# Performance work log

Hardware: AMD Instinct MI355X
Metric: run time of the kernel (lower is better)

Reference implementation:

```python
import jax, jax.numpy as jnp
import numpy as np
import math

B, S = 2, 2048
D_IN = 512
D_OUT = 512
P = 8
K = 8


def setup_inputs() -> dict:
    key = jax.random.key(0)
    ks = jax.random.split(key, 8)
    mean_phi = math.log(math.sqrt(2.0 / (D_IN * K)))
    mean_w2 = math.log(math.sqrt(2.0 / D_OUT))
    x = jax.random.normal(ks[0], (B, S, D_IN), dtype=jnp.float32)
    phi_raw = mean_phi + 0.2 * jax.random.normal(ks[1], (D_OUT, D_IN * K), dtype=jnp.float32)
    phi_bias = jnp.zeros((D_OUT,), dtype=jnp.float32)
    raw_weight2 = mean_w2 + 0.2 * jax.random.normal(ks[2], (P, D_OUT, D_OUT), dtype=jnp.float32)
    bias2 = jnp.zeros((P, D_OUT), dtype=jnp.float32)
    gate_raw2 = jnp.full((P,), -3.0, dtype=jnp.float32)
    # kaiming_uniform with a=sqrt(5) on shape (P, 2*D_in, D_out): fan_in = 2*D_in
    bound = math.sqrt(6.0 / ((1.0 + 5.0) * (2 * D_IN)))
    z_weight = jax.random.uniform(ks[3], (P, 2 * D_IN, D_OUT), dtype=jnp.float32,
                                  minval=-bound, maxval=bound)
    gate_raw = jnp.full((P,), -3.0, dtype=jnp.float32)
    output_bias = jnp.zeros((P, D_OUT), dtype=jnp.float32)
    return {
        "x": x, "phi_raw": phi_raw, "phi_bias": phi_bias,
        "raw_weight2": raw_weight2, "bias2": bias2, "gate_raw2": gate_raw2,
        "z_weight": z_weight, "gate_raw": gate_raw, "output_bias": output_bias,
    }


def reference(x, phi_raw, phi_bias, raw_weight2, bias2, gate_raw2,
              z_weight, gate_raw, output_bias):
    sp = jax.nn.softplus
    orig = x.shape
    x_flat = x.reshape(-1, D_IN)                              # [N, Din]
    N = x_flat.shape[0]
    shifts = jnp.linspace(-1.0, 1.0, K, dtype=x.dtype)        # [k]
    phi = sp(x_flat[:, :, None] + shifts[None, None, :])      # [N, Din, k]
    phi_flat = phi.reshape(N, D_IN * K)                       # [N, Din*k]
    # PositiveLinearHK: weight = softplus(raw)^2
    w_phi = jnp.square(sp(phi_raw))                           # [Dout, Din*k]
    x_proj = phi_flat @ w_phi.T + phi_bias                    # [N, Dout]
    g1 = jax.nn.sigmoid(gate_raw)[:, None, None]              # [P,1,1]
    z0 = sp(x_proj[None, :, :] * g1)                          # [P, N, Dout]
    w2 = jnp.square(sp(raw_weight2))                          # [P, Dout, Dout]
    # bmm(z0, w2.transpose(1,2)) == einsum over the second Dout axis of w2
    z1 = jnp.einsum('pnd,ped->pne', z0, w2) + bias2[:, None, :]
    g2 = jax.nn.sigmoid(gate_raw2)[:, None, None]
    z1 = sp(z1 * g2)                                          # [P, N, Dout]
    x_res_in = jnp.concatenate([x_flat, x_flat], axis=-1)     # [N, 2*Din]
    x_res = jnp.einsum('nc,pce->pne', x_res_in, z_weight)     # [P, N, Dout]
    z_final = sp(z1 + x_res) + output_bias[:, None, :]        # [P, N, Dout]
    out = jnp.transpose(z_final, (1, 0, 2))                   # [N, P, Dout]
    return out.reshape(tuple(orig[:-1]) + (P, D_OUT))
```

## Files before the change

### kernel.cpp

```cpp
#include <hip/hip_runtime.h>

typedef unsigned short u16;
typedef __attribute__((ext_vector_type(8))) short bf16x8;
typedef __attribute__((ext_vector_type(4))) float floatx4;
typedef __attribute__((ext_vector_type(8))) unsigned short u16x8;
typedef __attribute__((ext_vector_type(4))) unsigned short u16x4;

#define NTOK 4096
#define DDIN 512
#define DDOUT 512
#define NP 8
#define SPLITK 8

__device__ __forceinline__ float b2f(u16 b) {
    union { unsigned int u; float f; } v; v.u = ((unsigned int)b) << 16; return v.f;
}
__device__ __forceinline__ u16 f2b(float f) {
    union { float f; unsigned int u; } v; v.f = f;
    unsigned int r = (v.u + 0x7fffu + ((v.u >> 16) & 1u)) >> 16;
    return (u16)r;
}
__device__ __forceinline__ float sp(float x) {
    return fmaxf(x, 0.f) + __logf(1.f + __expf(-fabsf(x)));
}
__device__ __forceinline__ float sigm(float x) { return 1.f / (1.f + __expf(-x)); }

__device__ __forceinline__ void gld16(const u16* g, u16* l) {
    __builtin_amdgcn_global_load_lds((const __attribute__((address_space(1))) void*)g,
                                     (__attribute__((address_space(3))) void*)l, 16, 0, 0);
}

__global__ void prep_fused(const float* __restrict__ phi_raw, u16* __restrict__ wphi,
                           const float* __restrict__ raw_weight2, u16* __restrict__ w2b,
                           const float* __restrict__ x, u16* __restrict__ phi,
                           u16* __restrict__ xb,
                           const float* __restrict__ zw, u16* __restrict__ zwT) {
    const int b = blockIdx.x;
    const int t = threadIdx.x;
    if (b < 8192) {
        int i = b * 256 + t;
        float s = sp(phi_raw[i]);
        wphi[i] = f2b(s * s);
    } else if (b < 16384) {
        int i = (b - 8192) * 256 + t;
        float s = sp(raw_weight2[i]);
        w2b[i] = f2b(s * s);
    } else if (b < 24576) {
        int i = (b - 16384) * 256 + t;
        float xv = x[i];
        xb[i] = f2b(xv);
        u16x8 v;
#pragma unroll
        for (int k = 0; k < 8; ++k) {
            float s = -1.f + (2.f / 7.f) * (float)k;
            v[k] = f2b(sp(xv + s));
        }
        *(u16x8*)(phi + (size_t)i * 8) = v;
    } else {
        __shared__ float tb[32][33];
        int i = b - 24576;
        int p = i >> 8;
        int c0 = (i & 15) * 32, e0 = ((i >> 4) & 15) * 32;
        int tx = t & 31, ty = t >> 5;
        const float* base = zw + (size_t)p * 1024 * 512;
#pragma unroll
        for (int r = 0; r < 4; ++r) {
            int cl = ty * 4 + r;
            float a = base[(size_t)(c0 + cl) * 512 + e0 + tx];
            float bb = base[(size_t)(c0 + cl + 512) * 512 + e0 + tx];
            tb[cl][tx] = a + bb;
        }
        __syncthreads();
        u16* outb = zwT + (size_t)p * 512 * 512;
#pragma unroll
        for (int r = 0; r < 4; ++r) {
            int el = ty * 4 + r;
            outb[(size_t)(e0 + el) * 512 + c0 + tx] = f2b(tb[tx][el]);
        }
    }
}

__launch_bounds__(256, 3)
__global__ void gemm1p(const u16* __restrict__ phi, const u16* __restrict__ wphi,
                       u16* __restrict__ xpart) {
    __shared__ __align__(16) u16 lds[2 * 8192];
    u16* As = lds;
    u16* Bs = lds + 8192;

    const int id = blockIdx.x;
    const int kc = id & 7;
    const int local = id >> 3;
    const int o0 = (local & 3) * 128;
    const int n0 = (local >> 2) * 128;
    const int kbase = kc * 512;

    const int t = threadIdx.x;
    const int wave = t >> 6, lane = t & 63;
    const int wm = wave >> 1, wn = wave & 1;
    const int l15 = lane & 15, quad = lane >> 4;
    const int srow = t >> 3;
    const int sgx = (((t & 7) ^ (srow & 7))) * 8;

    floatx4 acc[4][4];
#pragma unroll
    for (int i = 0; i < 4; ++i)
#pragma unroll
        for (int j = 0; j < 4; ++j) acc[i][j] = {0.f, 0.f, 0.f, 0.f};

    for (int k0 = 0; k0 < 512; k0 += 64) {
        const u16* ga = phi + (size_t)(n0 + srow) * 4096 + kbase + k0 + sgx;
        const u16* gb = wphi + (size_t)(o0 + srow) * 4096 + kbase + k0 + sgx;
        __syncthreads();
#pragma unroll
        for (int c = 0; c < 4; ++c) {
            gld16(ga + (size_t)c * 32 * 4096, As + c * 2048 + t * 8);
            gld16(gb + (size_t)c * 32 * 4096, Bs + c * 2048 + t * 8);
        }
        __syncthreads();
#pragma unroll
        for (int ks = 0; ks < 2; ++ks) {
            bf16x8 a[4], b[4];
#pragma unroll
            for (int s = 0; s < 4; ++s) {
                int ra = wm * 64 + s * 16 + l15;
                int rb = wn * 64 + s * 16 + l15;
                a[s] = *(const bf16x8*)(As + ra * 64 + (((ks * 4 + quad) ^ (ra & 7)) * 8));
                b[s] = *(const bf16x8*)(Bs + rb * 64 + (((ks * 4 + quad) ^ (rb & 7)) * 8));
            }
#pragma unroll
            for (int sm = 0; sm < 4; ++sm)
#pragma unroll
                for (int sn = 0; sn < 4; ++sn)
                    acc[sm][sn] = __builtin_amdgcn_mfma_f32_16x16x32_bf16(a[sm], b[sn], acc[sm][sn], 0, 0, 0);
        }
    }

    u16* xp = xpart + (size_t)kc * NTOK * DDOUT;
#pragma unroll
    for (int sm = 0; sm < 4; ++sm)
#pragma unroll
        for (int sn = 0; sn < 4; ++sn) {
            int gcol = o0 + wn * 64 + sn * 16 + l15;
#pragma unroll
            for (int r = 0; r < 4; ++r) {
                int grow = n0 + wm * 64 + sm * 16 + quad * 4 + r;
                xp[(size_t)grow * DDOUT + gcol] = f2b(acc[sm][sn][r]);
            }
        }
}

__global__ void reduce_ep(const u16* __restrict__ xpart, const float* __restrict__ phi_bias,
                          const float* __restrict__ gate_raw, u16* __restrict__ z0) {
    int idx = blockIdx.x * 256 + threadIdx.x;
    int n = idx >> 7;
    int o4 = (idx & 127) * 4;
    size_t base = (size_t)n * DDOUT + o4;
    float s0 = 0.f, s1 = 0.f, s2 = 0.f, s3 = 0.f;
#pragma unroll
    for (int kc = 0; kc < SPLITK; ++kc) {
        u16x4 v = *(const u16x4*)(xpart + (size_t)kc * NTOK * DDOUT + base);
        s0 += b2f(v[0]); s1 += b2f(v[1]); s2 += b2f(v[2]); s3 += b2f(v[3]);
    }
    floatx4 pb = *(const floatx4*)(phi_bias + o4);
    s0 += pb[0]; s1 += pb[1]; s2 += pb[2]; s3 += pb[3];
#pragma unroll
    for (int p = 0; p < NP; ++p) {
        float g = sigm(gate_raw[p]);
        u16x4 v;
        v[0] = f2b(sp(s0 * g)); v[1] = f2b(sp(s1 * g));
        v[2] = f2b(sp(s2 * g)); v[3] = f2b(sp(s3 * g));
        *(u16x4*)(z0 + (size_t)p * NTOK * DDOUT + base) = v;
    }
}

__launch_bounds__(512, 2)
__global__ void gemm23(const u16* __restrict__ z0, const u16* __restrict__ w2b,
                       const u16* __restrict__ xb, const u16* __restrict__ zwT,
                       const float* __restrict__ bias2, const float* __restrict__ gate_raw2,
                       const float* __restrict__ output_bias, float* __restrict__ out) {
    __shared__ __align__(16) u16 lds[2 * 4 * 8192];

    const int id = blockIdx.x;
    const int p = id & 7;
    const int local = id >> 3;
    const int e0 = (local & 3) * 128;
    const int n0 = (local >> 2) * 128;

    const int t = threadIdx.x;
    const int wave = t >> 6, lane = t & 63;
    const int wm = wave & 1, wn = wave >> 1;
    const int l15 = lane & 15, quad = lane >> 4;
    const int srow = t >> 3;
    const int sgx = ((t & 7) ^ (srow & 7)) * 8;

    const u16* gA1 = z0  + (size_t)p * NTOK * DDOUT + (size_t)(n0 + srow) * 512 + sgx;
    const u16* gB1 = w2b + (size_t)p * DDOUT * DDOUT + (size_t)(e0 + srow) * 512 + sgx;
    const u16* gA2 = xb  + (size_t)(n0 + srow) * 512 + sgx;
    const u16* gB2 = zwT + (size_t)p * DDOUT * DDIN + (size_t)(e0 + srow) * 512 + sgx;

    floatx4 acc1[4][2], acc2[4][2];
#pragma unroll
    for (int i = 0; i < 4; ++i)
#pragma unroll
        for (int j = 0; j < 2; ++j) {
            acc1[i][j] = {0.f, 0.f, 0.f, 0.f};
            acc2[i][j] = {0.f, 0.f, 0.f, 0.f};
        }

    auto STAGE = [&](int b, int k0) {
        u16* L = lds + b * 32768;
#pragma unroll
        for (int c = 0; c < 2; ++c) {
            gld16(gA1 + k0 + c * 64 * 512, L + c * 4096 + t * 8);
            gld16(gB1 + k0 + c * 64 * 512, L + 8192 + c * 4096 + t * 8);
            gld16(gA2 + k0 + c * 64 * 512, L + 16384 + c * 4096 + t * 8);
            gld16(gB2 + k0 + c * 64 * 512, L + 24576 + c * 4096 + t * 8);
        }
    };

    STAGE(0, 0);
    for (int it = 0; it < 8; ++it) {
        const int cur = it & 1;
        __syncthreads();
        if (it < 7) STAGE(cur ^ 1, (it + 1) * 64);
        const u16* A1 = lds + cur * 32768;
        const u16* B1 = A1 + 8192;
        const u16* A2 = A1 + 16384;
        const u16* B2 = A1 + 24576;
#pragma unroll
        for (int ks = 0; ks < 2; ++ks) {
            bf16x8 a1[4], b1[2], a2[4], b2[2];
#pragma unroll
            for (int s = 0; s < 4; ++s) {
                int ra = wm * 64 + s * 16 + l15;
                int ko = ((ks * 4 + quad) ^ (ra & 7)) * 8;
                a1[s] = *(const bf16x8*)(A1 + ra * 64 + ko);
                a2[s] = *(const bf16x8*)(A2 + ra * 64 + ko);
            }
#pragma unroll
            for (int s = 0; s < 2; ++s) {
                int rb = wn * 32 + s * 16 + l15;
                int ko = ((ks * 4 + quad) ^ (rb & 7)) * 8;
                b1[s] = *(const bf16x8*)(B1 + rb * 64 + ko);
                b2[s] = *(const bf16x8*)(B2 + rb * 64 + ko);
            }
#pragma unroll
            for (int sm = 0; sm < 4; ++sm)
#pragma unroll
                for (int sn = 0; sn < 2; ++sn) {
                    acc1[sm][sn] = __builtin_amdgcn_mfma_f32_16x16x32_bf16(a1[sm], b1[sn], acc1[sm][sn], 0, 0, 0);
                    acc2[sm][sn] = __builtin_amdgcn_mfma_f32_16x16x32_bf16(a2[sm], b2[sn], acc2[sm][sn], 0, 0, 0);
                }
        }
    }

    const float g2p = sigm(gate_raw2[p]);
#pragma unroll
    for (int sm = 0; sm < 4; ++sm)
#pragma unroll
        for (int sn = 0; sn < 2; ++sn) {
            int gcol = e0 + wn * 32 + sn * 16 + l15;
            float bb = bias2[p * DDOUT + gcol];
            float ob = output_bias[p * DDOUT + gcol];
#pragma unroll
            for (int r = 0; r < 4; ++r) {
                int grow = n0 + wm * 64 + sm * 16 + quad * 4 + r;
                float v1 = acc1[sm][sn][r] + bb;
                float o = sp(sp(v1 * g2p) + acc2[sm][sn][r]) + ob;
                out[(size_t)grow * (NP * DDOUT) + p * DDOUT + gcol] = o;
            }
        }
}

extern "C" void kernel_launch(void* const* d_in, const int* in_sizes, int n_in,
                              void* d_out, int out_size, void* d_ws, size_t ws_size,
                              hipStream_t stream) {
    const float* x           = (const float*)d_in[0];
    const float* phi_raw     = (const float*)d_in[1];
    const float* phi_bias    = (const float*)d_in[2];
    const float* raw_weight2 = (const float*)d_in[3];
    const float* bias2       = (const float*)d_in[4];
    const float* gate_raw2   = (const float*)d_in[5];
    const float* z_weight    = (const float*)d_in[6];
    const float* gate_raw    = (const float*)d_in[7];
    const float* output_bias = (const float*)d_in[8];
    float* out = (float*)d_out;

    u16* ws   = (u16*)d_ws;
    u16* phi  = ws;
    u16* wphi = phi + (size_t)4096 * 4096;
    u16* w2b  = wphi + (size_t)512 * 4096;
    u16* zwT  = w2b + (size_t)8 * 512 * 512;
    u16* z0   = zwT + (size_t)8 * 512 * 512;
    u16* xb   = z0 + (size_t)8 * 4096 * 512;
    u16* xpart = (u16*)d_out;

    hipLaunchKernelGGL(prep_fused, dim3(26624), dim3(256), 0, stream,
                       phi_raw, wphi, raw_weight2, w2b, x, phi, xb, z_weight, zwT);
    hipLaunchKernelGGL(gemm1p, dim3(1024), dim3(256), 0, stream, phi, wphi, xpart);
    hipLaunchKernelGGL(reduce_ep, dim3(2048), dim3(256), 0, stream, xpart, phi_bias, gate_raw, z0);
    hipLaunchKernelGGL(gemm23, dim3(1024), dim3(512), 0, stream,
                       z0, w2b, xb, zwT, bias2, gate_raw2, output_bias, out);
}
```

Baseline: 216.6 us.

## Deepen gemm23 pipeline to four-stage K=32 ring with vmcnt waits, widen reduce

The fused second/residual GEMM moves from a double-buffered K=64 loop with __syncthreads to a four-buffer ring of K=32 stages. Loads run three stages ahead, and an explicit s_waitcnt vmcnt plus s_barrier replaces the full sync, so global-to-LDS copies overlap more MFMA work. LDS usage per block stays the same, and the swizzle is adapted to the 32-wide rows. The split-K reduction kernel now handles 8 elements per thread with 16-byte loads and stores and half the grid. The hand-written waitcnt counts must match the number of loads in flight, otherwise the kernel can read stale LDS data.

```diff
diff --git a/kernel.cpp b/kernel.cpp
--- a/kernel.cpp
+++ b/kernel.cpp
@@ -29,6 +29,11 @@
     __builtin_amdgcn_global_load_lds((const __attribute__((address_space(1))) void*)g,
                                      (__attribute__((address_space(3))) void*)l, 16, 0, 0);
 }
+
+#define WAITBAR(N) do { \
+    asm volatile("s_waitcnt vmcnt(" N ")\n\ts_barrier" ::: "memory"); \
+    __builtin_amdgcn_sched_barrier(0); \
+} while (0)
 
 __global__ void prep_fused(const float* __restrict__ phi_raw, u16* __restrict__ wphi,
                            const float* __restrict__ raw_weight2, u16* __restrict__ w2b,
@@ -152,24 +157,27 @@
 __global__ void reduce_ep(const u16* __restrict__ xpart, const float* __restrict__ phi_bias,
                           const float* __restrict__ gate_raw, u16* __restrict__ z0) {
     int idx = blockIdx.x * 256 + threadIdx.x;
-    int n = idx >> 7;
-    int o4 = (idx & 127) * 4;
-    size_t base = (size_t)n * DDOUT + o4;
-    float s0 = 0.f, s1 = 0.f, s2 = 0.f, s3 = 0.f;
+    int n = idx >> 6;
+    int o8 = (idx & 63) * 8;
+    size_t base = (size_t)n * DDOUT + o8;
+    float s[8];
+#pragma unroll
+    for (int j = 0; j < 8; ++j) s[j] = 0.f;
 #pragma unroll
     for (int kc = 0; kc < SPLITK; ++kc) {
-        u16x4 v = *(const u16x4*)(xpart + (size_t)kc * NTOK * DDOUT + base);
-        s0 += b2f(v[0]); s1 += b2f(v[1]); s2 += b2f(v[2]); s3 += b2f(v[3]);
-    }
-    floatx4 pb = *(const floatx4*)(phi_bias + o4);
-    s0 += pb[0]; s1 += pb[1]; s2 += pb[2]; s3 += pb[3];
+        u16x8 v = *(const u16x8*)(xpart + (size_t)kc * NTOK * DDOUT + base);
+#pragma unroll
+        for (int j = 0; j < 8; ++j) s[j] += b2f(v[j]);
+    }
+#pragma unroll
+    for (int j = 0; j < 8; ++j) s[j] += phi_bias[o8 + j];
 #pragma unroll
     for (int p = 0; p < NP; ++p) {
         float g = sigm(gate_raw[p]);
-        u16x4 v;
-        v[0] = f2b(sp(s0 * g)); v[1] = f2b(sp(s1 * g));
-        v[2] = f2b(sp(s2 * g)); v[3] = f2b(sp(s3 * g));
-        *(u16x4*)(z0 + (size_t)p * NTOK * DDOUT + base) = v;
+        u16x8 v;
+#pragma unroll
+        for (int j = 0; j < 8; ++j) v[j] = f2b(sp(s[j] * g));
+        *(u16x8*)(z0 + (size_t)p * NTOK * DDOUT + base) = v;
     }
 }
 
@@ -178,7 +186,7 @@
                        const u16* __restrict__ xb, const u16* __restrict__ zwT,
                        const float* __restrict__ bias2, const float* __restrict__ gate_raw2,
                        const float* __restrict__ output_bias, float* __restrict__ out) {
-    __shared__ __align__(16) u16 lds[2 * 4 * 8192];
+    __shared__ __align__(16) u16 lds[4 * 4 * 4096];
 
     const int id = blockIdx.x;
     const int p = id & 7;
@@ -190,8 +198,8 @@
     const int wave = t >> 6, lane = t & 63;
     const int wm = wave & 1, wn = wave >> 1;
     const int l15 = lane & 15, quad = lane >> 4;
-    const int srow = t >> 3;
-    const int sgx = ((t & 7) ^ (srow & 7)) * 8;
+    const int srow = t >> 2;
+    const int sgx = ((t & 3) ^ ((t >> 3) & 3)) * 8;
 
     const u16* gA1 = z0  + (size_t)p * NTOK * DDOUT + (size_t)(n0 + srow) * 512 + sgx;
     const u16* gB1 = w2b + (size_t)p * DDOUT * DDOUT + (size_t)(e0 + srow) * 512 + sgx;
@@ -208,50 +216,51 @@
         }
 
     auto STAGE = [&](int b, int k0) {
-        u16* L = lds + b * 32768;
-#pragma unroll
-        for (int c = 0; c < 2; ++c) {
-            gld16(gA1 + k0 + c * 64 * 512, L + c * 4096 + t * 8);
-            gld16(gB1 + k0 + c * 64 * 512, L + 8192 + c * 4096 + t * 8);
-            gld16(gA2 + k0 + c * 64 * 512, L + 16384 + c * 4096 + t * 8);
-            gld16(gB2 + k0 + c * 64 * 512, L + 24576 + c * 4096 + t * 8);
-        }
+        u16* L = lds + b * 16384;
+        gld16(gA1 + k0, L + t * 8);
+        gld16(gB1 + k0, L + 4096 + t * 8);
+        gld16(gA2 + k0, L + 8192 + t * 8);
+        gld16(gB2 + k0, L + 12288 + t * 8);
     };
 
+    const int ko = (quad ^ ((l15 >> 1) & 3)) * 8;
+
+    auto COMPUTE = [&](int b) {
+        const u16* A1 = lds + b * 16384;
+        const u16* B1 = A1 + 4096;
+        const u16* A2 = A1 + 8192;
+        const u16* B2 = A1 + 12288;
+        bf16x8 a1[4], b1[2], a2[4], b2[2];
+#pragma unroll
+        for (int s = 0; s < 4; ++s) {
+            int ra = wm * 64 + s * 16 + l15;
+            a1[s] = *(const bf16x8*)(A1 + ra * 32 + ko);
+            a2[s] = *(const bf16x8*)(A2 + ra * 32 + ko);
+        }
+#pragma unroll
+        for (int s = 0; s < 2; ++s) {
+            int rb = wn * 32 + s * 16 + l15;
+            b1[s] = *(const bf16x8*)(B1 + rb * 32 + ko);
+            b2[s] = *(const bf16x8*)(B2 + rb * 32 + ko);
+        }
+#pragma unroll
+        for (int sm = 0; sm < 4; ++sm)
+#pragma unroll
+            for (int sn = 0; sn < 2; ++sn) {
+                acc1[sm][sn] = __builtin_amdgcn_mfma_f32_16x16x32_bf16(a1[sm], b1[sn], acc1[sm][sn], 0, 0, 0);
+                acc2[sm][sn] = __builtin_amdgcn_mfma_f32_16x16x32_bf16(a2[sm], b2[sn], acc2[sm][sn], 0, 0, 0);
+            }
+    };
+
     STAGE(0, 0);
-    for (int it = 0; it < 8; ++it) {
-        const int cur = it & 1;
-        __syncthreads();
-        if (it < 7) STAGE(cur ^ 1, (it + 1) * 64);
-        const u16* A1 = lds + cur * 32768;
-        const u16* B1 = A1 + 8192;
-        const u16* A2 = A1 + 16384;
-        const u16* B2 = A1 + 24576;
-#pragma unroll
-        for (int ks = 0; ks < 2; ++ks) {
-            bf16x8 a1[4], b1[2], a2[4], b2[2];
-#pragma unroll
-            for (int s = 0; s < 4; ++s) {
-                int ra = wm * 64 + s * 16 + l15;
-                int ko = ((ks * 4 + quad) ^ (ra & 7)) * 8;
-                a1[s] = *(const bf16x8*)(A1 + ra * 64 + ko);
-                a2[s] = *(const bf16x8*)(A2 + ra * 64 + ko);
-            }
-#pragma unroll
-            for (int s = 0; s < 2; ++s) {
-                int rb = wn * 32 + s * 16 + l15;
-                int ko = ((ks * 4 + quad) ^ (rb & 7)) * 8;
-                b1[s] = *(const bf16x8*)(B1 + rb * 64 + ko);
-                b2[s] = *(const bf16x8*)(B2 + rb * 64 + ko);
-            }
-#pragma unroll
-            for (int sm = 0; sm < 4; ++sm)
-#pragma unroll
-                for (int sn = 0; sn < 2; ++sn) {
-                    acc1[sm][sn] = __builtin_amdgcn_mfma_f32_16x16x32_bf16(a1[sm], b1[sn], acc1[sm][sn], 0, 0, 0);
-                    acc2[sm][sn] = __builtin_amdgcn_mfma_f32_16x16x32_bf16(a2[sm], b2[sn], acc2[sm][sn], 0, 0, 0);
-                }
-        }
+    STAGE(1, 32);
+    STAGE(2, 64);
+    for (int it = 0; it < 16; ++it) {
+        if (it < 14) WAITBAR("8");
+        else if (it == 14) WAITBAR("4");
+        else WAITBAR("0");
+        if (it < 13) STAGE((it + 3) & 3, (it + 3) * 32);
+        COMPUTE(it & 3);
     }
 
     const float g2p = sigm(gate_raw2[p]);
@@ -298,7 +307,7 @@
     hipLaunchKernelGGL(prep_fused, dim3(26624), dim3(256), 0, stream,
                        phi_raw, wphi, raw_weight2, w2b, x, phi, xb, z_weight, zwT);
     hipLaunchKernelGGL(gemm1p, dim3(1024), dim3(256), 0, stream, phi, wphi, xpart);
-    hipLaunchKernelGGL(reduce_ep, dim3(2048), dim3(256), 0, stream, xpart, phi_bias, gate_raw, z0);
+    hipLaunchKernelGGL(reduce_ep, dim3(1024), dim3(256), 0, stream, xpart, phi_bias, gate_raw, z0);
     hipLaunchKernelGGL(gemm23, dim3(1024), dim3(512), 0, stream,
                        z0, w2b, xb, zwT, bias2, gate_raw2, output_bias, out);
 }
```

After: 225.7 us. +4.2%, slower.
